# Kernel tuning notes

Hardware: AMD Instinct MI355X
Metric: run time of the kernel (lower is better)

## Reference

```python
import jax, jax.numpy as jnp
import numpy as np

HIDDEN = 128
B, N, S = 4, 200, 512  # batch, 200 segments, 512 tokens each (hard-coded in source view())


def setup_inputs() -> dict:
    key = jax.random.key(0)
    ks = jax.random.split(key, 7)
    query = jax.random.normal(ks[0], (B, HIDDEN), dtype=jnp.float32)
    context = jax.random.normal(ks[1], (B, N, S, HIDDEN), dtype=jnp.float32)
    context_mask = jax.random.uniform(ks[2], (B, N, S), dtype=jnp.float32)
    scale = 1.0 / np.sqrt(HIDDEN)
    Wq = jax.random.normal(ks[3], (HIDDEN, HIDDEN), dtype=jnp.float32) * scale
    bq = jax.random.normal(ks[4], (HIDDEN,), dtype=jnp.float32) * 0.01
    Wc = jax.random.normal(ks[5], (HIDDEN, HIDDEN), dtype=jnp.float32) * scale
    bc = jax.random.normal(ks[6], (HIDDEN,), dtype=jnp.float32) * 0.01
    return {"query": query, "context": context, "context_mask": context_mask,
            "Wq": Wq, "bq": bq, "Wc": Wc, "bc": bc}


def reference(query, context, context_mask, Wq, bq, Wc, bc):
    # q_projection / c_projection (nn.Linear: x @ W.T + b)
    q = query @ Wq.T + bq                      # [B, H]
    c = context @ Wc.T + bc                    # [B, N, S, H]
    # bmm(reshape_c, q) -> scores [B, N, S]
    att = jnp.einsum('bnsh,bh->bns', c, q)
    masked_att = att * context_mask            # multiplicative mask (as in source)
    w = jax.nn.softmax(masked_att, axis=-1)    # [B, N, S]
    # fused dual-axis weighted reductions (avoid [B,N,S,H] broadcast materialization)
    result = jnp.einsum('bns,bnsh->bnh', w, context)       # sum over tokens S
    token_result = jnp.einsum('bns,bnsh->bsh', w, context)  # sum over segments N
    return (result, token_result)
```

## Files before the change

### kernel.cpp

```cpp
#include <hip/hip_runtime.h>
#include <hip/hip_bf16.h>
#include <math.h>

#define H    128
#define NB   4
#define NSEG 200
#define NS   512
#define GN   10
#define GS   64
#define NGRP (NSEG / GN)
#define NST  (NS / GS)


__global__ void precompute_kernel(const float* __restrict__ query,
                                  const float* __restrict__ Wq,
                                  const float* __restrict__ bq,
                                  const float* __restrict__ Wc,
                                  const float* __restrict__ bc,
                                  float* __restrict__ v_out,
                                  float* __restrict__ c0_out) {
    __shared__ float qsh[H];
    __shared__ float red[H];
    const int tid = threadIdx.x;
    const int b   = blockIdx.x;
    float acc = bq[tid];
    const float* qr = query + b * H;
    const float* wr = Wq + tid * H;
    for (int k = 0; k < H; ++k) acc += qr[k] * wr[k];
    qsh[tid] = acc;
    __syncthreads();
    float vacc = 0.f;
    for (int h2 = 0; h2 < H; ++h2) vacc += qsh[h2] * Wc[h2 * H + tid];
    v_out[b * H + tid] = vacc;
    red[tid] = qsh[tid] * bc[tid];
    __syncthreads();
    for (int off = H / 2; off > 0; off >>= 1) {
        if (tid < off) red[tid] += red[tid + off];
        __syncthreads();
    }
    if (tid == 0) c0_out[b] = red[0];
}

__global__ __launch_bounds__(512)
void scores_softmax_kernel(const float* __restrict__ context,
                           const float* __restrict__ mask,
                           const float* __restrict__ v,
                           const float* __restrict__ c0,
                           float* __restrict__ w_out) {
    __shared__ float4 vv4[32];
    __shared__ float  mk[NS];
    __shared__ float  sc[NS];
    __shared__ float  wred[8];

    const int tid = threadIdx.x;
    const int blk = blockIdx.x;
    const int b   = blk / NSEG;
    const float* cseg = context + (size_t)blk * NS * H;

    if (tid < 32) vv4[tid] = ((const float4*)(v + b * H))[tid];
    mk[tid] = mask[(size_t)blk * NS + tid];
    __syncthreads();

    const int   h4  = tid & 31;
    const int   rg  = tid >> 5;
    const float c0b = c0[b];

    #pragma unroll 4
    for (int it = 0; it < NS / 16; ++it) {
        const int s = it * 16 + rg;
        const float4 cv = ((const float4*)(cseg + (size_t)s * H))[h4];
        const float4 vq = vv4[h4];
        float p = cv.x * vq.x + cv.y * vq.y + cv.z * vq.z + cv.w * vq.w;
        p += __shfl_xor(p, 16);
        p += __shfl_xor(p, 8);
        p += __shfl_xor(p, 4);
        p += __shfl_xor(p, 2);
        p += __shfl_xor(p, 1);
        if (h4 == 0) sc[s] = (p + c0b) * mk[s];
    }
    __syncthreads();

    const float x = sc[tid];
    float m = x;
    for (int o = 32; o > 0; o >>= 1) m = fmaxf(m, __shfl_xor(m, o));
    const int wid = tid >> 6, lane = tid & 63;
    if (lane == 0) wred[wid] = m;
    __syncthreads();
    if (tid == 0) {
        float mm = wred[0];
        for (int i = 1; i < 8; ++i) mm = fmaxf(mm, wred[i]);
        wred[0] = mm;
    }
    __syncthreads();
    const float mx = wred[0];
    const float e  = __expf(x - mx);
    float ssum = e;
    for (int o = 32; o > 0; o >>= 1) ssum += __shfl_xor(ssum, o);
    __syncthreads();
    if (lane == 0) wred[wid] = ssum;
    __syncthreads();
    if (tid == 0) {
        float t = 0.f;
        for (int i = 0; i < 8; ++i) t += wred[i];
        wred[0] = t;
    }
    __syncthreads();
    w_out[(size_t)blk * NS + tid] = e / wred[0];
}

__global__ __launch_bounds__(512)
void weighted_kernel(const float* __restrict__ context,
                     const float* __restrict__ w,
                     float* __restrict__ result_part,
                     float* __restrict__ token_part) {
    const int bid = blockIdx.x;
    const int st  = bid & (NST - 1);
    const int tmp = bid / NST;
    const int ng  = tmp % NGRP;
    const int b   = tmp / NGRP;
    const int n0  = ng * GN;
    const int s0  = st * GS;

    const int tid = threadIdx.x;
    const int h4  = tid & 31;
    const int rg  = tid >> 5;

    __shared__ float  wt[GN * GS];
    __shared__ float4 red4[5 * 16 * 32];

    for (int i = tid; i < GN * GS; i += 512) {
        const int nn = i >> 6, ss = i & (GS - 1);
        wt[i] = w[((size_t)(b * NSEG + n0 + nn)) * NS + s0 + ss];
    }
    __syncthreads();

    float4 racc[GN];
    float4 tacc[4];
    #pragma unroll
    for (int n = 0; n < GN; ++n) racc[n] = make_float4(0.f, 0.f, 0.f, 0.f);
    #pragma unroll
    for (int j = 0; j < 4; ++j) tacc[j] = make_float4(0.f, 0.f, 0.f, 0.f);

    #pragma unroll
    for (int n = 0; n < GN; ++n) {
        const float* base = context + ((size_t)(b * NSEG + n0 + n) * NS + s0) * (size_t)H;
        #pragma unroll
        for (int j = 0; j < 4; ++j) {
            const int s = j * 16 + rg;
            const float  wv = wt[n * GS + s];
            const float4 cv = ((const float4*)(base + (size_t)s * H))[h4];
            racc[n].x += wv * cv.x; racc[n].y += wv * cv.y;
            racc[n].z += wv * cv.z; racc[n].w += wv * cv.w;
            tacc[j].x += wv * cv.x; tacc[j].y += wv * cv.y;
            tacc[j].z += wv * cv.z; tacc[j].w += wv * cv.w;
        }
    }

    #pragma unroll
    for (int j = 0; j < 4; ++j) {
        const int s = j * 16 + rg;
        ((float4*)token_part)[(((size_t)ng * NB + b) * NS + s0 + s) * 32 + h4] = tacc[j];
    }

    for (int nb = 0; nb < GN; nb += 5) {
        #pragma unroll
        for (int j = 0; j < 5; ++j)
            red4[(j * 16 + rg) * 32 + h4] = racc[nb + j];
        __syncthreads();
        for (int off = 8; off > 0; off >>= 1) {
            if (rg < off) {
                #pragma unroll
                for (int j = 0; j < 5; ++j) {
                    float4 o = red4[(j * 16 + rg + off) * 32 + h4];
                    float4 mm = red4[(j * 16 + rg) * 32 + h4];
                    mm.x += o.x; mm.y += o.y; mm.z += o.z; mm.w += o.w;
                    red4[(j * 16 + rg) * 32 + h4] = mm;
                }
            }
            __syncthreads();
        }
        if (rg == 0) {
            #pragma unroll
            for (int j = 0; j < 5; ++j)
                ((float4*)result_part)[(((size_t)(b * NSEG + n0 + nb + j)) * NST + st) * 32 + h4]
                    = red4[(j * 16) * 32 + h4];
        }
        __syncthreads();
    }
}

__global__ void combine_result_kernel(const float* __restrict__ part,
                                      float* __restrict__ out) {
    const int i = blockIdx.x * blockDim.x + threadIdx.x;
    const int row = i >> 5, h4 = i & 31;
    float4 acc = {0.f, 0.f, 0.f, 0.f};
    const float4* p = (const float4*)part;
    #pragma unroll
    for (int st = 0; st < NST; ++st) {
        float4 o = p[((size_t)row * NST + st) * 32 + h4];
        acc.x += o.x; acc.y += o.y; acc.z += o.z; acc.w += o.w;
    }
    ((float4*)out)[i] = acc;
}

__global__ void combine_token_kernel(const float* __restrict__ part,
                                     float* __restrict__ out) {
    const int i = blockIdx.x * blockDim.x + threadIdx.x;
    float4 acc = {0.f, 0.f, 0.f, 0.f};
    const float4* p = (const float4*)part;
    #pragma unroll
    for (int g = 0; g < NGRP; ++g) {
        float4 o = p[(size_t)g * (NB * NS * H / 4) + i];
        acc.x += o.x; acc.y += o.y; acc.z += o.z; acc.w += o.w;
    }
    ((float4*)out)[i] = acc;
}

extern "C" void kernel_launch(void* const* d_in, const int* in_sizes, int n_in,
                              void* d_out, int out_size, void* d_ws, size_t ws_size,
                              hipStream_t stream) {
    const float* query   = (const float*)d_in[0];
    const float* context = (const float*)d_in[1];
    const float* mask    = (const float*)d_in[2];
    const float* Wq      = (const float*)d_in[3];
    const float* bq      = (const float*)d_in[4];
    const float* Wc      = (const float*)d_in[5];
    const float* bc      = (const float*)d_in[6];

    float* out = (float*)d_out;
    float* wsf = (float*)d_ws;

    float* v     = wsf;
    float* c0    = wsf + 512;
    float* w     = wsf + 1024;
    float* rpart = wsf + 1024 + NB * NSEG * NS;
    float* tpart = rpart + NB * NSEG * NST * H;

    float* result_out = out;
    float* token_out  = out + NB * NSEG * H;

    precompute_kernel<<<NB, 128, 0, stream>>>(query, Wq, bq, Wc, bc, v, c0);
    scores_softmax_kernel<<<NB * NSEG, 512, 0, stream>>>(context, mask, v, c0, w);
    weighted_kernel<<<NB * NGRP * NST, 512, 0, stream>>>(context, w, rpart, tpart);
    combine_result_kernel<<<NB * NSEG * H / 4 / 256, 256, 0, stream>>>(rpart, result_out);
    combine_token_kernel<<<NB * NS * H / 4 / 256, 256, 0, stream>>>(tpart, token_out);
}
```

Baseline: 353.8 us.

## Fuse projection into scores kernel, merge combine kernels, halve weighted tile

The separate query-projection kernel is removed and its work is done redundantly inside every scores/softmax block, which drops one launch at the cost of recomputing two 128x128 matvecs per block. The two combine kernels become one launch covering both outputs. The weighted kernel moves to 256 threads with a 32-token tile, which doubles the block count and the result partials that have to be combined.

Result: no change. 359.3 us (+1.6%).

```diff
diff --git a/kernel.cpp b/kernel.cpp
--- a/kernel.cpp
+++ b/kernel.cpp
@@ -7,63 +7,58 @@
 #define NSEG 200
 #define NS   512
 #define GN   10
-#define GS   64
+#define GS   32
 #define NGRP (NSEG / GN)
 #define NST  (NS / GS)
 
-
-__global__ void precompute_kernel(const float* __restrict__ query,
-                                  const float* __restrict__ Wq,
-                                  const float* __restrict__ bq,
-                                  const float* __restrict__ Wc,
-                                  const float* __restrict__ bc,
-                                  float* __restrict__ v_out,
-                                  float* __restrict__ c0_out) {
-    __shared__ float qsh[H];
-    __shared__ float red[H];
-    const int tid = threadIdx.x;
-    const int b   = blockIdx.x;
-    float acc = bq[tid];
-    const float* qr = query + b * H;
-    const float* wr = Wq + tid * H;
-    for (int k = 0; k < H; ++k) acc += qr[k] * wr[k];
-    qsh[tid] = acc;
-    __syncthreads();
-    float vacc = 0.f;
-    for (int h2 = 0; h2 < H; ++h2) vacc += qsh[h2] * Wc[h2 * H + tid];
-    v_out[b * H + tid] = vacc;
-    red[tid] = qsh[tid] * bc[tid];
-    __syncthreads();
-    for (int off = H / 2; off > 0; off >>= 1) {
-        if (tid < off) red[tid] += red[tid + off];
-        __syncthreads();
-    }
-    if (tid == 0) c0_out[b] = red[0];
-}
 
 __global__ __launch_bounds__(512)
 void scores_softmax_kernel(const float* __restrict__ context,
                            const float* __restrict__ mask,
-                           const float* __restrict__ v,
-                           const float* __restrict__ c0,
+                           const float* __restrict__ query,
+                           const float* __restrict__ Wq,
+                           const float* __restrict__ bq,
+                           const float* __restrict__ Wc,
+                           const float* __restrict__ bc,
                            float* __restrict__ w_out) {
+    __shared__ float  qsh[H];
     __shared__ float4 vv4[32];
     __shared__ float  mk[NS];
     __shared__ float  sc[NS];
     __shared__ float  wred[8];
+    __shared__ float  c0sh;
 
     const int tid = threadIdx.x;
     const int blk = blockIdx.x;
     const int b   = blk / NSEG;
     const float* cseg = context + (size_t)blk * NS * H;
 
-    if (tid < 32) vv4[tid] = ((const float4*)(v + b * H))[tid];
+    if (tid < H) {
+        float acc = bq[tid];
+        const float* qr = query + b * H;
+        const float* wr = Wq + tid * H;
+        #pragma unroll 4
+        for (int k = 0; k < H; ++k) acc += qr[k] * wr[k];
+        qsh[tid] = acc;
+    }
     mk[tid] = mask[(size_t)blk * NS + tid];
+    __syncthreads();
+    if (tid < H) {
+        float vacc = 0.f;
+        #pragma unroll 4
+        for (int h2 = 0; h2 < H; ++h2) vacc += qsh[h2] * Wc[h2 * H + tid];
+        ((float*)vv4)[tid] = vacc;
+    }
+    if (tid < 64) {
+        float p = qsh[tid] * bc[tid] + qsh[tid + 64] * bc[tid + 64];
+        for (int o = 32; o > 0; o >>= 1) p += __shfl_xor(p, o);
+        if (tid == 0) c0sh = p;
+    }
     __syncthreads();
 
     const int   h4  = tid & 31;
     const int   rg  = tid >> 5;
-    const float c0b = c0[b];
+    const float c0b = c0sh;
 
     #pragma unroll 4
     for (int it = 0; it < NS / 16; ++it) {
@@ -108,7 +103,7 @@
     w_out[(size_t)blk * NS + tid] = e / wred[0];
 }
 
-__global__ __launch_bounds__(512)
+__global__ __launch_bounds__(256)
 void weighted_kernel(const float* __restrict__ context,
                      const float* __restrict__ w,
                      float* __restrict__ result_part,
@@ -126,10 +121,10 @@
     const int rg  = tid >> 5;
 
     __shared__ float  wt[GN * GS];
-    __shared__ float4 red4[5 * 16 * 32];
-
-    for (int i = tid; i < GN * GS; i += 512) {
-        const int nn = i >> 6, ss = i & (GS - 1);
+    __shared__ float4 red4[5 * 8 * 32];
+
+    for (int i = tid; i < GN * GS; i += 256) {
+        const int nn = i >> 5, ss = i & (GS - 1);
         wt[i] = w[((size_t)(b * NSEG + n0 + nn)) * NS + s0 + ss];
     }
     __syncthreads();
@@ -146,7 +141,7 @@
         const float* base = context + ((size_t)(b * NSEG + n0 + n) * NS + s0) * (size_t)H;
         #pragma unroll
         for (int j = 0; j < 4; ++j) {
-            const int s = j * 16 + rg;
+            const int s = j * 8 + rg;
             const float  wv = wt[n * GS + s];
             const float4 cv = ((const float4*)(base + (size_t)s * H))[h4];
             racc[n].x += wv * cv.x; racc[n].y += wv * cv.y;
@@ -158,23 +153,23 @@
 
     #pragma unroll
     for (int j = 0; j < 4; ++j) {
-        const int s = j * 16 + rg;
+        const int s = j * 8 + rg;
         ((float4*)token_part)[(((size_t)ng * NB + b) * NS + s0 + s) * 32 + h4] = tacc[j];
     }
 
     for (int nb = 0; nb < GN; nb += 5) {
         #pragma unroll
         for (int j = 0; j < 5; ++j)
-            red4[(j * 16 + rg) * 32 + h4] = racc[nb + j];
+            red4[(j * 8 + rg) * 32 + h4] = racc[nb + j];
         __syncthreads();
-        for (int off = 8; off > 0; off >>= 1) {
+        for (int off = 4; off > 0; off >>= 1) {
             if (rg < off) {
                 #pragma unroll
                 for (int j = 0; j < 5; ++j) {
-                    float4 o = red4[(j * 16 + rg + off) * 32 + h4];
-                    float4 mm = red4[(j * 16 + rg) * 32 + h4];
+                    float4 o = red4[(j * 8 + rg + off) * 32 + h4];
+                    float4 mm = red4[(j * 8 + rg) * 32 + h4];
                     mm.x += o.x; mm.y += o.y; mm.z += o.z; mm.w += o.w;
-                    red4[(j * 16 + rg) * 32 + h4] = mm;
+                    red4[(j * 8 + rg) * 32 + h4] = mm;
                 }
             }
             __syncthreads();
@@ -183,37 +178,39 @@
             #pragma unroll
             for (int j = 0; j < 5; ++j)
                 ((float4*)result_part)[(((size_t)(b * NSEG + n0 + nb + j)) * NST + st) * 32 + h4]
-                    = red4[(j * 16) * 32 + h4];
+                    = red4[(j * 8) * 32 + h4];
         }
         __syncthreads();
     }
 }
 
-__global__ void combine_result_kernel(const float* __restrict__ part,
-                                      float* __restrict__ out) {
-    const int i = blockIdx.x * blockDim.x + threadIdx.x;
-    const int row = i >> 5, h4 = i & 31;
-    float4 acc = {0.f, 0.f, 0.f, 0.f};
-    const float4* p = (const float4*)part;
-    #pragma unroll
-    for (int st = 0; st < NST; ++st) {
-        float4 o = p[((size_t)row * NST + st) * 32 + h4];
-        acc.x += o.x; acc.y += o.y; acc.z += o.z; acc.w += o.w;
-    }
-    ((float4*)out)[i] = acc;
-}
-
-__global__ void combine_token_kernel(const float* __restrict__ part,
-                                     float* __restrict__ out) {
-    const int i = blockIdx.x * blockDim.x + threadIdx.x;
-    float4 acc = {0.f, 0.f, 0.f, 0.f};
-    const float4* p = (const float4*)part;
-    #pragma unroll
-    for (int g = 0; g < NGRP; ++g) {
-        float4 o = p[(size_t)g * (NB * NS * H / 4) + i];
-        acc.x += o.x; acc.y += o.y; acc.z += o.z; acc.w += o.w;
-    }
-    ((float4*)out)[i] = acc;
+__global__ __launch_bounds__(256)
+void combine_kernel(const float* __restrict__ rpart,
+                    const float* __restrict__ tpart,
+                    float* __restrict__ out) {
+    const int RQ = NB * NSEG * H / 4;
+    const int i  = blockIdx.x * 256 + threadIdx.x;
+    if (i < RQ) {
+        const int row = i >> 5, h4 = i & 31;
+        float4 acc = {0.f, 0.f, 0.f, 0.f};
+        const float4* p = (const float4*)rpart;
+        #pragma unroll
+        for (int st = 0; st < NST; ++st) {
+            float4 o = p[((size_t)row * NST + st) * 32 + h4];
+            acc.x += o.x; acc.y += o.y; acc.z += o.z; acc.w += o.w;
+        }
+        ((float4*)out)[i] = acc;
+    } else {
+        const int j = i - RQ;
+        float4 acc = {0.f, 0.f, 0.f, 0.f};
+        const float4* p = (const float4*)tpart;
+        #pragma unroll
+        for (int g = 0; g < NGRP; ++g) {
+            float4 o = p[(size_t)g * (NB * NS * H / 4) + j];
+            acc.x += o.x; acc.y += o.y; acc.z += o.z; acc.w += o.w;
+        }
+        ((float4*)out)[i] = acc;
+    }
 }
 
 extern "C" void kernel_launch(void* const* d_in, const int* in_sizes, int n_in,
@@ -230,18 +227,13 @@
     float* out = (float*)d_out;
     float* wsf = (float*)d_ws;
 
-    float* v     = wsf;
-    float* c0    = wsf + 512;
-    float* w     = wsf + 1024;
-    float* rpart = wsf + 1024 + NB * NSEG * NS;
+    float* w     = wsf;
+    float* rpart = wsf + NB * NSEG * NS;
     float* tpart = rpart + NB * NSEG * NST * H;
 
-    float* result_out = out;
-    float* token_out  = out + NB * NSEG * H;
-
-    precompute_kernel<<<NB, 128, 0, stream>>>(query, Wq, bq, Wc, bc, v, c0);
-    scores_softmax_kernel<<<NB * NSEG, 512, 0, stream>>>(context, mask, v, c0, w);
-    weighted_kernel<<<NB * NGRP * NST, 512, 0, stream>>>(context, w, rpart, tpart);
-    combine_result_kernel<<<NB * NSEG * H / 4 / 256, 256, 0, stream>>>(rpart, result_out);
-    combine_token_kernel<<<NB * NS * H / 4 / 256, 256, 0, stream>>>(tpart, token_out);
-}
+    scores_softmax_kernel<<<NB * NSEG, 512, 0, stream>>>(
+        context, mask, query, Wq, bq, Wc, bc, w);
+    weighted_kernel<<<NB * NGRP * NST, 256, 0, stream>>>(context, w, rpart, tpart);
+    const int total4 = NB * NSEG * H / 4 + NB * NS * H / 4;
+    combine_kernel<<<total4 / 256, 256, 0, stream>>>(rpart, tpart, out);
+}
```
